# Kernel optimization log

Hardware: AMD Instinct MI355X
Metric: run time of the kernel (lower is better)

## Reference

```python
import jax, jax.numpy as jnp
import numpy as np

EPS = 1e-6
NEG = -1e9
RES_RATIO = 1.0  # res_ratio init arg
MAKE_SYM = True


def _ln(x, g, b):
    m = jnp.mean(x, axis=-1, keepdims=True)
    v = jnp.mean((x - m) ** 2, axis=-1, keepdims=True)
    return (x - m) * jax.lax.rsqrt(v + EPS) * g + b


def _sim(q, k, W1q, W1k, b1, W2, b2):
    # NN(concat([q,k])) with first dense split into query/key halves:
    # relu(q@W1q + k@W1k + b1) @ W2 + b2  -> avoids materializing the 2d concat.
    qa = q @ W1q  # [b,n,sq,h]
    kb = k @ W1k  # [b,n,sk,h]
    h1 = jax.nn.relu(qa[:, :, :, None, :] + kb[:, :, None, :, :] + b1)  # [b,n,sq,sk,h]
    s = jnp.einsum('bnqkh,h->bnqk', h1, W2[:, 0]) + b2[0]
    if MAKE_SYM:
        qb = q @ W1k
        ka = k @ W1q
        h2 = jax.nn.relu(ka[:, :, None, :, :] + qb[:, :, :, None, :] + b1)
        s = s + jnp.einsum('bnqkh,h->bnqk', h2, W2[:, 0]) + b2[0]
    return s


def _attention(v, k, q, mask, Ww, bw, Wd, bd, W1q, W1k, b1, W2, b2):
    q = q @ Ww + bw
    k = k @ Ww + bw
    v = v @ Ww + bw
    logits = _sim(q, k, W1q, W1k, b1, W2, b2)
    if mask is not None:
        logits = logits + mask * NEG
    attn = jax.nn.softmax(logits, axis=-1)
    out = jnp.einsum('bnqk,bnkd->bnqd', attn, v)
    return out @ Wd + bd, attn


def setup_inputs() -> dict:
    key = jax.random.key(0)
    B, N, S, D, DFF, H = 4, 1, 256, 128, 512, 128
    ks = jax.random.split(key, 16)
    s = 0.02
    inp = {
        'x': jax.random.normal(ks[0], (B, N, S, D), jnp.float32),
        'enc_output': jax.random.normal(ks[1], (B, N, S, D), jnp.float32),
        'com_mask': jnp.zeros((B, N, S, S), jnp.float32),
        'dec_mask': jnp.zeros((B, N, S, S), jnp.float32),
        # shared pairwise-score MLP NN: Dense(H, relu) -> Dense(1)
        'W1q': jax.random.normal(ks[2], (D, H), jnp.float32) * s,
        'W1k': jax.random.normal(ks[3], (D, H), jnp.float32) * s,
        'b1': jnp.zeros((H,), jnp.float32),
        'W2': jax.random.normal(ks[4], (H, 1), jnp.float32) * s,
        'b2': jnp.zeros((1,), jnp.float32),
        # mha1 projections
        'Ww1': jax.random.normal(ks[5], (D, D), jnp.float32) * s,
        'bw1': jnp.zeros((D,), jnp.float32),
        'Wd1': jax.random.normal(ks[6], (D, D), jnp.float32) * s,
        'bd1': jnp.zeros((D,), jnp.float32),
        # mha2 projections
        'Ww2': jax.random.normal(ks[7], (D, D), jnp.float32) * s,
        'bw2': jnp.zeros((D,), jnp.float32),
        'Wd2': jax.random.normal(ks[8], (D, D), jnp.float32) * s,
        'bd2': jnp.zeros((D,), jnp.float32),
        # ffn
        'Wf1': jax.random.normal(ks[9], (D, DFF), jnp.float32) * s,
        'bf1': jnp.zeros((DFF,), jnp.float32),
        'Wf2': jax.random.normal(ks[10], (DFF, D), jnp.float32) * s,
        'bf2': jnp.zeros((D,), jnp.float32),
        # layernorms
        'ln1_g': jnp.ones((D,), jnp.float32), 'ln1_b': jnp.zeros((D,), jnp.float32),
        'ln2_g': jnp.ones((D,), jnp.float32), 'ln2_b': jnp.zeros((D,), jnp.float32),
        'ln3_g': jnp.ones((D,), jnp.float32), 'ln3_b': jnp.zeros((D,), jnp.float32),
    }
    return inp


def reference(x, enc_output, com_mask, dec_mask,
              W1q, W1k, b1, W2, b2,
              Ww1, bw1, Wd1, bd1,
              Ww2, bw2, Wd2, bd2,
              Wf1, bf1, Wf2, bf2,
              ln1_g, ln1_b, ln2_g, ln2_b, ln3_g, ln3_b):
    r = RES_RATIO
    # self-attention block (dropout inactive, eval mode)
    attn1, aw1 = _attention(x, x, x, com_mask, Ww1, bw1, Wd1, bd1, W1q, W1k, b1, W2, b2)
    out1 = _ln((2 - r) * attn1 + r * x, ln1_g, ln1_b)
    # cross-attention block
    attn2, aw2 = _attention(enc_output, enc_output, out1, dec_mask, Ww2, bw2, Wd2, bd2, W1q, W1k, b1, W2, b2)
    out2 = _ln((2 - r) * attn2 + r * out1, ln2_g, ln2_b)
    # ffn
    ffn = jax.nn.relu(out2 @ Wf1 + bf1) @ Wf2 + bf2
    out3 = _ln((2 - r) * ffn + r * out2, ln3_g, ln3_b)
    return out3
```

## Files before the change

kernel.cpp:

```cpp
#include <hip/hip_runtime.h>
#include <math.h>


#define LN_EPS 1e-6f
#define NEGV  (-1e9f)

constexpr int B = 4, S = 256, D = 128, H = 128, DFF = 512;
constexpr int R = B * S;

struct P {
    const float *x, *enc, *com_mask, *dec_mask;
    const float *W1q, *W1k, *b1, *W2;
    const float *Ww1, *bw1, *Wd1, *bd1;
    const float *Ww2, *bw2, *Wd2, *bd2;
    const float *Wf1, *bf1, *Wf2, *bf2;
    const float *ln1g, *ln1b, *ln2g, *ln2b, *ln3g, *ln3b;
    float *out;
    float *xw, *qa, *kb, *kv2w, *kb2, *ka2;
};

__global__ __launch_bounds__(512) void proj3_kernel(P p)
{
    const int g = blockIdx.y, tid = threadIdx.x;
    const int r0 = blockIdx.x * 4;
    __shared__ __align__(16) float Ash[4 * 128];
    __shared__ __align__(16) float Pw[4 * 128];
    __shared__ __align__(16) float Pp[4 * 4 * 128];
    __shared__ __align__(16) float P2[2 * 2 * 4 * 128];

    const float* A    = g ? p.enc  : p.x;
    const float* Wp   = g ? p.Ww2  : p.Ww1;
    const float* bp   = g ? p.bw2  : p.bw1;
    float*       o_w  = g ? p.kv2w : p.xw;
    const float* Wsec = g ? p.W1k  : p.W1q;
    const float* bsec = g ? nullptr: p.b1;
    float*       o_s  = g ? p.kb2  : p.qa;
    const float* Wthr = g ? p.W1q  : p.W1k;
    float*       o_t  = g ? p.ka2  : p.kb;

    if (tid < 128)
        ((float4*)Ash)[tid] = ((const float4*)(A + (size_t)r0 * 128))[tid];
    __syncthreads();

    {
        const int kh = tid >> 7, unit = tid & 127, lr = unit >> 5, c4 = unit & 31;
        const float4* W4 = (const float4*)Wp;
        float4 acc = (kh == 0) ? ((const float4*)bp)[c4] : make_float4(0.f, 0.f, 0.f, 0.f);
        const int k0 = kh * 32;
        #pragma unroll 8
        for (int k = 0; k < 32; ++k) {
            const float a = Ash[lr * 128 + k0 + k];
            const float4 w = W4[(k0 + k) * 32 + c4];
            acc.x = fmaf(a, w.x, acc.x); acc.y = fmaf(a, w.y, acc.y);
            acc.z = fmaf(a, w.z, acc.z); acc.w = fmaf(a, w.w, acc.w);
        }
        ((float4*)Pp)[kh * 128 + unit] = acc;
    }
    __syncthreads();
    if (tid < 128) {
        const int lr = tid >> 5, c4 = tid & 31;
        const float4 a0 = ((const float4*)Pp)[tid];
        const float4 a1 = ((const float4*)Pp)[128 + tid];
        const float4 a2 = ((const float4*)Pp)[256 + tid];
        const float4 a3 = ((const float4*)Pp)[384 + tid];
        const float4 w = make_float4(a0.x + a1.x + a2.x + a3.x,
                                     a0.y + a1.y + a2.y + a3.y,
                                     a0.z + a1.z + a2.z + a3.z,
                                     a0.w + a1.w + a2.w + a3.w);
        ((float4*)Pw)[tid] = w;
        ((float4*)o_w)[(size_t)(r0 + lr) * 32 + c4] = w;
    }
    __syncthreads();

    {
        const int which = tid >> 8, sub = tid & 255;
        const int kh = sub >> 7, unit2 = sub & 127, lr = unit2 >> 5, c4 = unit2 & 31;
        const float* W = which ? Wthr : Wsec;
        const float* bb = which ? nullptr : bsec;
        const float4* W4 = (const float4*)W;
        float4 acc = (kh == 0 && bb) ? ((const float4*)bb)[c4]
                                     : make_float4(0.f, 0.f, 0.f, 0.f);
        const int k0 = kh * 64;
        #pragma unroll 8
        for (int k = 0; k < 64; ++k) {
            const float a = Pw[lr * 128 + k0 + k];
            const float4 w = W4[(k0 + k) * 32 + c4];
            acc.x = fmaf(a, w.x, acc.x); acc.y = fmaf(a, w.y, acc.y);
            acc.z = fmaf(a, w.z, acc.z); acc.w = fmaf(a, w.w, acc.w);
        }
        ((float4*)P2)[(which * 2 + kh) * 128 + unit2] = acc;
    }
    __syncthreads();
    if (tid < 256) {
        const int which = tid >> 7, unit2 = tid & 127;
        const int lr = unit2 >> 5, c4 = unit2 & 31;
        const float4 p0 = ((const float4*)P2)[(which * 2 + 0) * 128 + unit2];
        const float4 p1 = ((const float4*)P2)[(which * 2 + 1) * 128 + unit2];
        float* o = which ? o_t : o_s;
        ((float4*)o)[(size_t)(r0 + lr) * 32 + c4] =
            make_float4(p0.x + p1.x, p0.y + p1.y, p0.z + p1.z, p0.w + p1.w);
    }
}

#define SC8(ACC, O1, X1, O2, X2)                                               \
    ACC = fmaf(fmaxf((O1).x + (X1).x, 0.f), w.x, ACC);                         \
    ACC = fmaf(fmaxf((O1).y + (X1).y, 0.f), w.y, ACC);                         \
    ACC = fmaf(fmaxf((O1).z + (X1).z, 0.f), w.z, ACC);                         \
    ACC = fmaf(fmaxf((O1).w + (X1).w, 0.f), w.w, ACC);                         \
    ACC = fmaf(fmaxf((O2).x + (X2).x, 0.f), w.x, ACC);                         \
    ACC = fmaf(fmaxf((O2).y + (X2).y, 0.f), w.y, ACC);                         \
    ACC = fmaf(fmaxf((O2).z + (X2).z, 0.f), w.z, ACC);                         \
    ACC = fmaf(fmaxf((O2).w + (X2).w, 0.f), w.w, ACC);

template<bool FIRST>
__device__ __forceinline__ void attn_stage(const P& p, float* smem,
                                           int tid, int r0, int bS)
{
    float* s8    = smem;
    float* rowS  = smem + 1024;
    float* rinvS = smem + 1536;
    float* qa2L  = smem + 1552;
    float* qb2L  = smem + 2064;
    constexpr int SB = 2576;

    const float* __restrict__ S1g = FIRST ? p.kb : p.kb2;
    const float* __restrict__ S2g = FIRST ? p.qa : p.ka2;
    const float* mask = FIRST ? p.com_mask : p.dec_mask;
    const float* V    = FIRST ? p.xw : p.kv2w;
    const float* Wd   = FIRST ? p.Wd1 : p.Wd2;
    const float* bd   = FIRST ? p.bd1 : p.bd2;
    const float* lg   = FIRST ? p.ln1g : p.ln2g;
    const float* lb   = FIRST ? p.ln1b : p.ln2b;

    {
        const int hh = tid & 7, unit = tid >> 3, kk = unit & 31, rg = unit >> 5;
        const int rA = r0 + 2 * rg, rB = rA + 1;

        float4 o1A[4], o1B[4], o2A[4], o2B[4], w2r[4];
        #pragma unroll
        for (int j = 0; j < 4; ++j) {
            const int h = hh * 4 + 32 * j;
            if (FIRST) {
                o1A[j] = *(const float4*)(p.qa + (size_t)rA * H + h);
                o1B[j] = *(const float4*)(p.qa + (size_t)rB * H + h);
                o2A[j] = *(const float4*)(p.kb + (size_t)rA * H + h);
                o2B[j] = *(const float4*)(p.kb + (size_t)rB * H + h);
            } else {
                o1A[j] = *(const float4*)(qa2L + (2 * rg) * H + h);
                o1B[j] = *(const float4*)(qa2L + (2 * rg + 1) * H + h);
                o2A[j] = *(const float4*)(qb2L + (2 * rg) * H + h);
                o2B[j] = *(const float4*)(qb2L + (2 * rg + 1) * H + h);
            }
            w2r[j] = *(const float4*)(p.W2 + h);
        }

        #pragma unroll
        for (int kt = 0; kt < 4; ++kt) {
            const float* __restrict__ r1a = S1g + (size_t)(bS + kt * 64 + kk)      * H;
            const float* __restrict__ r1b = S1g + (size_t)(bS + kt * 64 + kk + 32) * H;
            const float* __restrict__ r2a = S2g + (size_t)(bS + kt * 64 + kk)      * H;
            const float* __restrict__ r2b = S2g + (size_t)(bS + kt * 64 + kk + 32) * H;

            float4 x1a[4], x1b[4], x2a[4], x2b[4];
            #pragma unroll
            for (int j = 0; j < 4; ++j) {
                const int h = hh * 4 + 32 * j;
                x1a[j] = *(const float4*)(r1a + h);
                x1b[j] = *(const float4*)(r1b + h);
                x2a[j] = *(const float4*)(r2a + h);
                x2b[j] = *(const float4*)(r2b + h);
            }

            float aAa = 0.f, aAb = 0.f, aBa = 0.f, aBb = 0.f;
            #pragma unroll
            for (int j = 0; j < 4; ++j) {
                const float4 w = w2r[j];
                SC8(aAa, o1A[j], x1a[j], o2A[j], x2a[j])
                SC8(aAb, o1A[j], x1b[j], o2A[j], x2b[j])
                SC8(aBa, o1B[j], x1a[j], o2B[j], x2a[j])
                SC8(aBb, o1B[j], x1b[j], o2B[j], x2b[j])
            }
            #pragma unroll
            for (int o = 1; o < 8; o <<= 1) {
                aAa += __shfl_xor(aAa, o, 8);
                aAb += __shfl_xor(aAb, o, 8);
                aBa += __shfl_xor(aBa, o, 8);
                aBb += __shfl_xor(aBb, o, 8);
            }
            if (hh == 0) {
                const int k = kt * 64 + kk;
                s8[(2 * rg) * 256 + k]          = aAa + mask[(size_t)rA * S + k] * NEGV;
                s8[(2 * rg) * 256 + k + 32]     = aAb + mask[(size_t)rA * S + k + 32] * NEGV;
                s8[(2 * rg + 1) * 256 + k]      = aBa + mask[(size_t)rB * S + k] * NEGV;
                s8[(2 * rg + 1) * 256 + k + 32] = aBb + mask[(size_t)rB * S + k + 32] * NEGV;
            }
        }
    }
    __syncthreads();

    {
        const int g = tid >> 6, c = tid & 63;
        if (g < 4) {
            float* rowp = s8 + g * 256;
            float m = -INFINITY;
            #pragma unroll
            for (int k = c; k < 256; k += 64) m = fmaxf(m, rowp[k]);
            for (int o = 32; o; o >>= 1) m = fmaxf(m, __shfl_xor(m, o, 64));
            float s = 0.f;
            #pragma unroll
            for (int k = c; k < 256; k += 64) { const float e = __expf(rowp[k] - m); rowp[k] = e; s += e; }
            for (int o = 32; o; o >>= 1) s += __shfl_xor(s, o, 64);
            if (c == 0) rinvS[g] = 1.f / s;
        }
    }
    __syncthreads();

    float* avp = smem + SB;
    float* aoS = smem + SB + 2048;
    float* pp  = smem + SB + 2560;

    {
        const int r = tid >> 7, t = tid & 127, kq = t >> 5, c4 = t & 31;
        const float4* V4 = (const float4*)(V + (size_t)bS * D);
        const float* sp = s8 + r * 256 + kq * 64;
        float4 acc = make_float4(0.f, 0.f, 0.f, 0.f);
        #pragma unroll 8
        for (int k = 0; k < 64; ++k) {
            const float a = sp[k];
            const float4 v = V4[(kq * 64 + k) * 32 + c4];
            acc.x = fmaf(a, v.x, acc.x); acc.y = fmaf(a, v.y, acc.y);
            acc.z = fmaf(a, v.z, acc.z); acc.w = fmaf(a, v.w, acc.w);
        }
        ((float4*)avp)[(r * 4 + kq) * 32 + c4] = acc;
    }
    __syncthreads();
    if (tid < 128) {
        const int r = tid >> 5, c4 = tid & 31;
        float4 s0 = ((const float4*)avp)[(r * 4 + 0) * 32 + c4];
        const float4 s1 = ((const float4*)avp)[(r * 4 + 1) * 32 + c4];
        const float4 s2 = ((const float4*)avp)[(r * 4 + 2) * 32 + c4];
        const float4 s3 = ((const float4*)avp)[(r * 4 + 3) * 32 + c4];
        const float rv = rinvS[r];
        ((float4*)aoS)[r * 32 + c4] = make_float4(
            (s0.x + s1.x + s2.x + s3.x) * rv, (s0.y + s1.y + s2.y + s3.y) * rv,
            (s0.z + s1.z + s2.z + s3.z) * rv, (s0.w + s1.w + s2.w + s3.w) * rv);
    }
    __syncthreads();

    {
        const int kq = tid >> 7, unit = tid & 127, r = unit >> 5, c4 = unit & 31;
        const float4* W4 = (const float4*)Wd;
        const float* ap = aoS + r * 128 + kq * 32;
        float4 acc = make_float4(0.f, 0.f, 0.f, 0.f);
        #pragma unroll 8
        for (int k = 0; k < 32; ++k) {
            const float a = ap[k];
            const float4 w = W4[(kq * 32 + k) * 32 + c4];
            acc.x = fmaf(a, w.x, acc.x); acc.y = fmaf(a, w.y, acc.y);
            acc.z = fmaf(a, w.z, acc.z); acc.w = fmaf(a, w.w, acc.w);
        }
        ((float4*)pp)[kq * 128 + unit] = acc;
    }
    __syncthreads();

    if (tid < 128) {
        const int r = tid >> 5, c4 = tid & 31;
        const float4 p0 = ((const float4*)pp)[tid];
        const float4 p1 = ((const float4*)pp)[128 + tid];
        const float4 p2 = ((const float4*)pp)[256 + tid];
        const float4 p3 = ((const float4*)pp)[384 + tid];
        const float4 bv0 = ((const float4*)bd)[c4];
        float4 r4;
        if (FIRST) r4 = ((const float4*)(p.x + (size_t)(r0 + r) * 128))[c4];
        else       r4 = ((const float4*)rowS)[r * 32 + c4];
        const float x0 = p0.x + p1.x + p2.x + p3.x + bv0.x + r4.x;
        const float x1 = p0.y + p1.y + p2.y + p3.y + bv0.y + r4.y;
        const float x2 = p0.z + p1.z + p2.z + p3.z + bv0.z + r4.z;
        const float x3 = p0.w + p1.w + p2.w + p3.w + bv0.w + r4.w;
        float s  = x0 + x1 + x2 + x3;
        float s2 = x0 * x0 + x1 * x1 + x2 * x2 + x3 * x3;
        for (int o = 16; o; o >>= 1) { s += __shfl_xor(s, o, 32); s2 += __shfl_xor(s2, o, 32); }
        const float m = s * (1.f / 128), var = s2 * (1.f / 128) - m * m;
        const float rs = rsqrtf(var + LN_EPS);
        const float4 gv = ((const float4*)lg)[c4], bv = ((const float4*)lb)[c4];
        float4 o4;
        o4.x = (x0 - m) * rs * gv.x + bv.x; o4.y = (x1 - m) * rs * gv.y + bv.y;
        o4.z = (x2 - m) * rs * gv.z + bv.z; o4.w = (x3 - m) * rs * gv.w + bv.w;
        ((float4*)rowS)[r * 32 + c4] = o4;
    }
    __syncthreads();

    if (FIRST) {
        float* qpp  = smem + SB;
        float* q2wS = smem + SB + 2048;
        float* qp2  = smem + SB + 2560;
        {
            const int kq = tid >> 7, unit = tid & 127, r = unit >> 5, c4 = unit & 31;
            const float4* W4 = (const float4*)p.Ww2;
            const float* ap = rowS + r * 128 + kq * 32;
            float4 acc = make_float4(0.f, 0.f, 0.f, 0.f);
            #pragma unroll 8
            for (int k = 0; k < 32; ++k) {
                const float a = ap[k];
                const float4 w = W4[(kq * 32 + k) * 32 + c4];
                acc.x = fmaf(a, w.x, acc.x); acc.y = fmaf(a, w.y, acc.y);
                acc.z = fmaf(a, w.z, acc.z); acc.w = fmaf(a, w.w, acc.w);
            }
            ((float4*)qpp)[kq * 128 + unit] = acc;
        }
        __syncthreads();
        if (tid < 128) {
            const int c4 = tid & 31;
            const float4 p0 = ((const float4*)qpp)[tid];
            const float4 p1 = ((const float4*)qpp)[128 + tid];
            const float4 p2 = ((const float4*)qpp)[256 + tid];
            const float4 p3 = ((const float4*)qpp)[384 + tid];
            const float4 bw = ((const float4*)p.bw2)[c4];
            ((float4*)q2wS)[tid] = make_float4(p0.x + p1.x + p2.x + p3.x + bw.x,
                                               p0.y + p1.y + p2.y + p3.y + bw.y,
                                               p0.z + p1.z + p2.z + p3.z + bw.z,
                                               p0.w + p1.w + p2.w + p3.w + bw.w);
        }
        __syncthreads();
        {
            const int which = tid >> 8, sub = tid & 255;
            const int kh = sub >> 7, unit2 = sub & 127;
            const float4* W4 = (const float4*)(which ? p.W1k : p.W1q);
            const int r = unit2 >> 5;
            const float* ap = q2wS + r * 128 + kh * 64;
            float4 acc = make_float4(0.f, 0.f, 0.f, 0.f);
            #pragma unroll 8
            for (int k = 0; k < 64; ++k) {
                const float a = ap[k];
                const float4 w = W4[(kh * 64 + k) * 32 + (unit2 & 31)];
                acc.x = fmaf(a, w.x, acc.x); acc.y = fmaf(a, w.y, acc.y);
                acc.z = fmaf(a, w.z, acc.z); acc.w = fmaf(a, w.w, acc.w);
            }
            ((float4*)qp2)[(which * 2 + kh) * 128 + unit2] = acc;
        }
        __syncthreads();
        if (tid < 256) {
            const int which = tid >> 7, unit2 = tid & 127;
            const int c4 = unit2 & 31;
            const float4 p0 = ((const float4*)qp2)[(which * 2 + 0) * 128 + unit2];
            const float4 p1 = ((const float4*)qp2)[(which * 2 + 1) * 128 + unit2];
            const float4 b1v = ((const float4*)p.b1)[c4];
            float* oq = which ? qb2L : qa2L;
            ((float4*)oq)[unit2] =
                make_float4(p0.x + p1.x + b1v.x, p0.y + p1.y + b1v.y,
                            p0.z + p1.z + b1v.z, p0.w + p1.w + b1v.w);
        }
        __syncthreads();
    } else {
        float* hidP = smem + SB;
        float* part = smem + SB + 8192;
        {
            const int c = tid & 127, kh = tid >> 7;
            const float4* Wf1_4 = (const float4*)p.Wf1;
            float4 a0 = make_float4(0.f,0.f,0.f,0.f), a1 = a0, a2 = a0, a3 = a0;
            const int kbase = kh * 32;
            #pragma unroll 8
            for (int k = 0; k < 32; ++k) {
                const int kk = kbase + k;
                const float4 w = Wf1_4[kk * 128 + c];
                const float s0 = rowS[kk],       s1 = rowS[128 + kk];
                const float s2 = rowS[256 + kk], s3 = rowS[384 + kk];
                a0.x=fmaf(s0,w.x,a0.x); a0.y=fmaf(s0,w.y,a0.y); a0.z=fmaf(s0,w.z,a0.z); a0.w=fmaf(s0,w.w,a0.w);
                a1.x=fmaf(s1,w.x,a1.x); a1.y=fmaf(s1,w.y,a1.y); a1.z=fmaf(s1,w.z,a1.z); a1.w=fmaf(s1,w.w,a1.w);
                a2.x=fmaf(s2,w.x,a2.x); a2.y=fmaf(s2,w.y,a2.y); a2.z=fmaf(s2,w.z,a2.z); a2.w=fmaf(s2,w.w,a2.w);
                a3.x=fmaf(s3,w.x,a3.x); a3.y=fmaf(s3,w.y,a3.y); a3.z=fmaf(s3,w.z,a3.z); a3.w=fmaf(s3,w.w,a3.w);
            }
            float4* h4 = (float4*)hidP;
            const int base = kh * 512;
            h4[base + 0*128 + c] = a0; h4[base + 1*128 + c] = a1;
            h4[base + 2*128 + c] = a2; h4[base + 3*128 + c] = a3;
        }
        __syncthreads();
        for (int i = tid; i < 2048; i += 512) {
            hidP[i] = fmaxf(hidP[i] + hidP[2048 + i] + hidP[4096 + i] + hidP[6144 + i]
                            + p.bf1[i & 511], 0.f);
        }
        __syncthreads();
        {
            const int c4f = tid & 31, kg = tid >> 5;
            const float4* Wf2_4 = (const float4*)p.Wf2;
            float4 a0 = make_float4(0.f,0.f,0.f,0.f), a1 = a0, a2 = a0, a3 = a0;
            const int kbase = kg * 32;
            const float* h0 = hidP + 0 * 512 + kbase;
            const float* h1 = hidP + 1 * 512 + kbase;
            const float* h2 = hidP + 2 * 512 + kbase;
            const float* h3 = hidP + 3 * 512 + kbase;
            #pragma unroll 8
            for (int k = 0; k < 32; ++k) {
                const float4 w = Wf2_4[(kbase + k) * 32 + c4f];
                const float s0 = h0[k], s1 = h1[k], s2 = h2[k], s3 = h3[k];
                a0.x=fmaf(s0,w.x,a0.x); a0.y=fmaf(s0,w.y,a0.y); a0.z=fmaf(s0,w.z,a0.z); a0.w=fmaf(s0,w.w,a0.w);
                a1.x=fmaf(s1,w.x,a1.x); a1.y=fmaf(s1,w.y,a1.y); a1.z=fmaf(s1,w.z,a1.z); a1.w=fmaf(s1,w.w,a1.w);
                a2.x=fmaf(s2,w.x,a2.x); a2.y=fmaf(s2,w.y,a2.y); a2.z=fmaf(s2,w.z,a2.z); a2.w=fmaf(s2,w.w,a2.w);
                a3.x=fmaf(s3,w.x,a3.x); a3.y=fmaf(s3,w.y,a3.y); a3.z=fmaf(s3,w.z,a3.z); a3.w=fmaf(s3,w.w,a3.w);
            }
            float4* p4 = (float4*)part;
            p4[kg * 128 + 0 * 32 + c4f] = a0; p4[kg * 128 + 1 * 32 + c4f] = a1;
            p4[kg * 128 + 2 * 32 + c4f] = a2; p4[kg * 128 + 3 * 32 + c4f] = a3;
        }
        __syncthreads();
        if (tid < 128) {
            const int r = tid >> 5, c4 = tid & 31;
            const float4* p4 = (const float4*)part;
            float4 sum = ((const float4*)p.bf2)[c4];
            #pragma unroll
            for (int kg = 0; kg < 16; ++kg) {
                const float4 v = p4[kg * 128 + r * 32 + c4];
                sum.x += v.x; sum.y += v.y; sum.z += v.z; sum.w += v.w;
            }
            const float4 r4 = ((const float4*)rowS)[r * 32 + c4];
            const float x0 = sum.x + r4.x, x1 = sum.y + r4.y;
            const float x2 = sum.z + r4.z, x3 = sum.w + r4.w;
            float s  = x0 + x1 + x2 + x3;
            float s2 = x0 * x0 + x1 * x1 + x2 * x2 + x3 * x3;
            for (int o = 16; o; o >>= 1) { s += __shfl_xor(s, o, 32); s2 += __shfl_xor(s2, o, 32); }
            const float m = s * (1.f / 128), var = s2 * (1.f / 128) - m * m;
            const float rs = rsqrtf(var + LN_EPS);
            const float4 gv = ((const float4*)p.ln3g)[c4], bv = ((const float4*)p.ln3b)[c4];
            float4 o4;
            o4.x = (x0 - m) * rs * gv.x + bv.x; o4.y = (x1 - m) * rs * gv.y + bv.y;
            o4.z = (x2 - m) * rs * gv.z + bv.z; o4.w = (x3 - m) * rs * gv.w + bv.w;
            ((float4*)p.out)[(size_t)(r0 + r) * 32 + c4] = o4;
        }
    }
}

__global__ __launch_bounds__(512) void fused_attn12_kernel(P p)
{
    __shared__ __align__(16) float smem[18960];
    const int tid = threadIdx.x;
    const int r0 = blockIdx.x * 4, bS = (r0 >> 8) * S;
    attn_stage<true >(p, smem, tid, r0, bS);
    attn_stage<false>(p, smem, tid, r0, bS);
}

extern "C" void kernel_launch(void* const* d_in, const int* in_sizes, int n_in,
                              void* d_out, int out_size, void* d_ws, size_t ws_size,
                              hipStream_t stream) {
    (void)in_sizes; (void)n_in; (void)out_size; (void)ws_size;
    P p;
    p.x        = (const float*)d_in[0];
    p.enc      = (const float*)d_in[1];
    p.com_mask = (const float*)d_in[2];
    p.dec_mask = (const float*)d_in[3];
    p.W1q = (const float*)d_in[4];
    p.W1k = (const float*)d_in[5];
    p.b1  = (const float*)d_in[6];
    p.W2  = (const float*)d_in[7];
    p.Ww1 = (const float*)d_in[9];
    p.bw1 = (const float*)d_in[10];
    p.Wd1 = (const float*)d_in[11];
    p.bd1 = (const float*)d_in[12];
    p.Ww2 = (const float*)d_in[13];
    p.bw2 = (const float*)d_in[14];
    p.Wd2 = (const float*)d_in[15];
    p.bd2 = (const float*)d_in[16];
    p.Wf1 = (const float*)d_in[17];
    p.bf1 = (const float*)d_in[18];
    p.Wf2 = (const float*)d_in[19];
    p.bf2 = (const float*)d_in[20];
    p.ln1g = (const float*)d_in[21];
    p.ln1b = (const float*)d_in[22];
    p.ln2g = (const float*)d_in[23];
    p.ln2b = (const float*)d_in[24];
    p.ln3g = (const float*)d_in[25];
    p.ln3b = (const float*)d_in[26];
    p.out  = (float*)d_out;

    float* ws = (float*)d_ws;
    const size_t RD = (size_t)R * D;
    p.xw    = ws;
    p.qa    = p.xw    + RD;
    p.kb    = p.qa    + RD;
    p.kv2w  = p.kb    + RD;
    p.kb2   = p.kv2w  + RD;
    p.ka2   = p.kb2   + RD;

    proj3_kernel<<<dim3(R / 4, 2), 512, 0, stream>>>(p);
    fused_attn12_kernel<<<R / 4, 512, 0, stream>>>(p);
}
```

Before: 166.1 us.

## Split fused attention kernel into separate score and tail kernels

Splits the single fused two-stage attention kernel into four launches: a score kernel for each attention stage that splits the key dimension across two blocks, and a tail kernel for softmax, PV, projection and LayerNorm. Intermediates (scores, out1, qa2/qb2) now go through global workspace instead of shared memory. The aim is more parallelism for the pairwise-MLP score computation and smaller shared-memory footprints for better occupancy. The cost is extra launches and global round trips for the score matrix and intermediates.

```diff
diff --git a/kernel.cpp b/kernel.cpp
--- a/kernel.cpp
+++ b/kernel.cpp
@@ -16,7 +16,7 @@
     const float *Wf1, *bf1, *Wf2, *bf2;
     const float *ln1g, *ln1b, *ln2g, *ln2b, *ln3g, *ln3b;
     float *out;
-    float *xw, *qa, *kb, *kv2w, *kb2, *ka2;
+    float *xw, *qa, *kb, *kv2w, *kb2, *ka2, *qa2, *qb2, *out1, *sbuf;
 };
 
 __global__ __launch_bounds__(512) void proj3_kernel(P p)
@@ -113,89 +113,96 @@
     ACC = fmaf(fmaxf((O2).w + (X2).w, 0.f), w.w, ACC);
 
 template<bool FIRST>
-__device__ __forceinline__ void attn_stage(const P& p, float* smem,
-                                           int tid, int r0, int bS)
+__global__ __launch_bounds__(512) void score_kernel(P p)
 {
+    const int tid = threadIdx.x;
+    const int r0 = blockIdx.y * 4, bS = (r0 >> 8) * S;
+    const int k0 = blockIdx.x * 128;
+
+    const float* __restrict__ O1g = FIRST ? p.qa : p.qa2;
+    const float* __restrict__ O2g = FIRST ? p.kb : p.qb2;
+    const float* __restrict__ S1g = FIRST ? p.kb : p.kb2;
+    const float* __restrict__ S2g = FIRST ? p.qa : p.ka2;
+    const float* mask = FIRST ? p.com_mask : p.dec_mask;
+
+    const int hh = tid & 7, unit = tid >> 3, kk = unit & 31, rg = unit >> 5;
+    const int rA = r0 + 2 * rg, rB = rA + 1;
+
+    float4 o1A[4], o1B[4], o2A[4], o2B[4], w2r[4];
+    #pragma unroll
+    for (int j = 0; j < 4; ++j) {
+        const int h = hh * 4 + 32 * j;
+        o1A[j] = *(const float4*)(O1g + (size_t)rA * H + h);
+        o1B[j] = *(const float4*)(O1g + (size_t)rB * H + h);
+        o2A[j] = *(const float4*)(O2g + (size_t)rA * H + h);
+        o2B[j] = *(const float4*)(O2g + (size_t)rB * H + h);
+        w2r[j] = *(const float4*)(p.W2 + h);
+    }
+
+    #pragma unroll
+    for (int kt = 0; kt < 2; ++kt) {
+        const int kbase = k0 + kt * 64;
+        const float* __restrict__ r1a = S1g + (size_t)(bS + kbase + kk)      * H;
+        const float* __restrict__ r1b = S1g + (size_t)(bS + kbase + kk + 32) * H;
+        const float* __restrict__ r2a = S2g + (size_t)(bS + kbase + kk)      * H;
+        const float* __restrict__ r2b = S2g + (size_t)(bS + kbase + kk + 32) * H;
+
+        float4 x1a[4], x1b[4], x2a[4], x2b[4];
+        #pragma unroll
+        for (int j = 0; j < 4; ++j) {
+            const int h = hh * 4 + 32 * j;
+            x1a[j] = *(const float4*)(r1a + h);
+            x1b[j] = *(const float4*)(r1b + h);
+            x2a[j] = *(const float4*)(r2a + h);
+            x2b[j] = *(const float4*)(r2b + h);
+        }
+
+        float aAa = 0.f, aAb = 0.f, aBa = 0.f, aBb = 0.f;
+        #pragma unroll
+        for (int j = 0; j < 4; ++j) {
+            const float4 w = w2r[j];
+            SC8(aAa, o1A[j], x1a[j], o2A[j], x2a[j])
+            SC8(aAb, o1A[j], x1b[j], o2A[j], x2b[j])
+            SC8(aBa, o1B[j], x1a[j], o2B[j], x2a[j])
+            SC8(aBb, o1B[j], x1b[j], o2B[j], x2b[j])
+        }
+        #pragma unroll
+        for (int o = 1; o < 8; o <<= 1) {
+            aAa += __shfl_xor(aAa, o, 8);
+            aAb += __shfl_xor(aAb, o, 8);
+            aBa += __shfl_xor(aBa, o, 8);
+            aBb += __shfl_xor(aBb, o, 8);
+        }
+        if (hh == 0) {
+            const int ka = kbase + kk, kbi = kbase + kk + 32;
+            p.sbuf[(size_t)rA * S + ka]  = aAa + mask[(size_t)rA * S + ka]  * NEGV;
+            p.sbuf[(size_t)rA * S + kbi] = aAb + mask[(size_t)rA * S + kbi] * NEGV;
+            p.sbuf[(size_t)rB * S + ka]  = aBa + mask[(size_t)rB * S + ka]  * NEGV;
+            p.sbuf[(size_t)rB * S + kbi] = aBb + mask[(size_t)rB * S + kbi] * NEGV;
+        }
+    }
+}
+
+template<bool FIRST>
+__global__ __launch_bounds__(512) void tail_kernel(P p)
+{
+    __shared__ __align__(16) float smem[FIRST ? 6160 : 17936];
     float* s8    = smem;
     float* rowS  = smem + 1024;
     float* rinvS = smem + 1536;
-    float* qa2L  = smem + 1552;
-    float* qb2L  = smem + 2064;
-    constexpr int SB = 2576;
-
-    const float* __restrict__ S1g = FIRST ? p.kb : p.kb2;
-    const float* __restrict__ S2g = FIRST ? p.qa : p.ka2;
-    const float* mask = FIRST ? p.com_mask : p.dec_mask;
-    const float* V    = FIRST ? p.xw : p.kv2w;
-    const float* Wd   = FIRST ? p.Wd1 : p.Wd2;
-    const float* bd   = FIRST ? p.bd1 : p.bd2;
-    const float* lg   = FIRST ? p.ln1g : p.ln2g;
-    const float* lb   = FIRST ? p.ln1b : p.ln2b;
-
-    {
-        const int hh = tid & 7, unit = tid >> 3, kk = unit & 31, rg = unit >> 5;
-        const int rA = r0 + 2 * rg, rB = rA + 1;
-
-        float4 o1A[4], o1B[4], o2A[4], o2B[4], w2r[4];
-        #pragma unroll
-        for (int j = 0; j < 4; ++j) {
-            const int h = hh * 4 + 32 * j;
-            if (FIRST) {
-                o1A[j] = *(const float4*)(p.qa + (size_t)rA * H + h);
-                o1B[j] = *(const float4*)(p.qa + (size_t)rB * H + h);
-                o2A[j] = *(const float4*)(p.kb + (size_t)rA * H + h);
-                o2B[j] = *(const float4*)(p.kb + (size_t)rB * H + h);
-            } else {
-                o1A[j] = *(const float4*)(qa2L + (2 * rg) * H + h);
-                o1B[j] = *(const float4*)(qa2L + (2 * rg + 1) * H + h);
-                o2A[j] = *(const float4*)(qb2L + (2 * rg) * H + h);
-                o2B[j] = *(const float4*)(qb2L + (2 * rg + 1) * H + h);
-            }
-            w2r[j] = *(const float4*)(p.W2 + h);
-        }
-
-        #pragma unroll
-        for (int kt = 0; kt < 4; ++kt) {
-            const float* __restrict__ r1a = S1g + (size_t)(bS + kt * 64 + kk)      * H;
-            const float* __restrict__ r1b = S1g + (size_t)(bS + kt * 64 + kk + 32) * H;
-            const float* __restrict__ r2a = S2g + (size_t)(bS + kt * 64 + kk)      * H;
-            const float* __restrict__ r2b = S2g + (size_t)(bS + kt * 64 + kk + 32) * H;
-
-            float4 x1a[4], x1b[4], x2a[4], x2b[4];
-            #pragma unroll
-            for (int j = 0; j < 4; ++j) {
-                const int h = hh * 4 + 32 * j;
-                x1a[j] = *(const float4*)(r1a + h);
-                x1b[j] = *(const float4*)(r1b + h);
-                x2a[j] = *(const float4*)(r2a + h);
-                x2b[j] = *(const float4*)(r2b + h);
-            }
-
-            float aAa = 0.f, aAb = 0.f, aBa = 0.f, aBb = 0.f;
-            #pragma unroll
-            for (int j = 0; j < 4; ++j) {
-                const float4 w = w2r[j];
-                SC8(aAa, o1A[j], x1a[j], o2A[j], x2a[j])
-                SC8(aAb, o1A[j], x1b[j], o2A[j], x2b[j])
-                SC8(aBa, o1B[j], x1a[j], o2B[j], x2a[j])
-                SC8(aBb, o1B[j], x1b[j], o2B[j], x2b[j])
-            }
-            #pragma unroll
-            for (int o = 1; o < 8; o <<= 1) {
-                aAa += __shfl_xor(aAa, o, 8);
-                aAb += __shfl_xor(aAb, o, 8);
-                aBa += __shfl_xor(aBa, o, 8);
-                aBb += __shfl_xor(aBb, o, 8);
-            }
-            if (hh == 0) {
-                const int k = kt * 64 + kk;
-                s8[(2 * rg) * 256 + k]          = aAa + mask[(size_t)rA * S + k] * NEGV;
-                s8[(2 * rg) * 256 + k + 32]     = aAb + mask[(size_t)rA * S + k + 32] * NEGV;
-                s8[(2 * rg + 1) * 256 + k]      = aBa + mask[(size_t)rB * S + k] * NEGV;
-                s8[(2 * rg + 1) * 256 + k + 32] = aBb + mask[(size_t)rB * S + k + 32] * NEGV;
-            }
-        }
-    }
+    constexpr int SB = 1552;
+
+    const int tid = threadIdx.x;
+    const int r0 = blockIdx.x * 4, bS = (r0 >> 8) * S;
+
+    const float* V  = FIRST ? p.xw : p.kv2w;
+    const float* Wd = FIRST ? p.Wd1 : p.Wd2;
+    const float* bd = FIRST ? p.bd1 : p.bd2;
+    const float* lg = FIRST ? p.ln1g : p.ln2g;
+    const float* lb = FIRST ? p.ln1b : p.ln2b;
+
+    for (int i = tid; i < 1024; i += 512)
+        s8[i] = p.sbuf[(size_t)(r0 + (i >> 8)) * S + (i & 255)];
     __syncthreads();
 
     {
@@ -270,9 +277,8 @@
         const float4 p2 = ((const float4*)pp)[256 + tid];
         const float4 p3 = ((const float4*)pp)[384 + tid];
         const float4 bv0 = ((const float4*)bd)[c4];
-        float4 r4;
-        if (FIRST) r4 = ((const float4*)(p.x + (size_t)(r0 + r) * 128))[c4];
-        else       r4 = ((const float4*)rowS)[r * 32 + c4];
+        const float* res = FIRST ? p.x : p.out1;
+        const float4 r4 = ((const float4*)(res + (size_t)(r0 + r) * 128))[c4];
         const float x0 = p0.x + p1.x + p2.x + p3.x + bv0.x + r4.x;
         const float x1 = p0.y + p1.y + p2.y + p3.y + bv0.y + r4.y;
         const float x2 = p0.z + p1.z + p2.z + p3.z + bv0.z + r4.z;
@@ -287,6 +293,7 @@
         o4.x = (x0 - m) * rs * gv.x + bv.x; o4.y = (x1 - m) * rs * gv.y + bv.y;
         o4.z = (x2 - m) * rs * gv.z + bv.z; o4.w = (x3 - m) * rs * gv.w + bv.w;
         ((float4*)rowS)[r * 32 + c4] = o4;
+        if (FIRST) ((float4*)p.out1)[(size_t)(r0 + r) * 32 + c4] = o4;
     }
     __syncthreads();
 
@@ -341,16 +348,15 @@
         __syncthreads();
         if (tid < 256) {
             const int which = tid >> 7, unit2 = tid & 127;
-            const int c4 = unit2 & 31;
+            const int r = unit2 >> 5, c4 = unit2 & 31;
             const float4 p0 = ((const float4*)qp2)[(which * 2 + 0) * 128 + unit2];
             const float4 p1 = ((const float4*)qp2)[(which * 2 + 1) * 128 + unit2];
             const float4 b1v = ((const float4*)p.b1)[c4];
-            float* oq = which ? qb2L : qa2L;
-            ((float4*)oq)[unit2] =
+            float* oq = which ? p.qb2 : p.qa2;
+            ((float4*)oq)[(size_t)(r0 + r) * 32 + c4] =
                 make_float4(p0.x + p1.x + b1v.x, p0.y + p1.y + b1v.y,
                             p0.z + p1.z + b1v.z, p0.w + p1.w + b1v.w);
         }
-        __syncthreads();
     } else {
         float* hidP = smem + SB;
         float* part = smem + SB + 8192;
@@ -428,15 +434,6 @@
             ((float4*)p.out)[(size_t)(r0 + r) * 32 + c4] = o4;
         }
     }
-}
-
-__global__ __launch_bounds__(512) void fused_attn12_kernel(P p)
-{
-    __shared__ __align__(16) float smem[18960];
-    const int tid = threadIdx.x;
-    const int r0 = blockIdx.x * 4, bS = (r0 >> 8) * S;
-    attn_stage<true >(p, smem, tid, r0, bS);
-    attn_stage<false>(p, smem, tid, r0, bS);
 }
 
 extern "C" void kernel_launch(void* const* d_in, const int* in_sizes, int n_in,
@@ -473,14 +470,21 @@
     p.out  = (float*)d_out;
 
     float* ws = (float*)d_ws;
-    const size_t RD = (size_t)R * D;
+    const size_t RD  = (size_t)R * D;
     p.xw    = ws;
     p.qa    = p.xw    + RD;
     p.kb    = p.qa    + RD;
     p.kv2w  = p.kb    + RD;
     p.kb2   = p.kv2w  + RD;
     p.ka2   = p.kb2   + RD;
+    p.qa2   = p.ka2   + RD;
+    p.qb2   = p.qa2   + RD;
+    p.out1  = p.qb2   + RD;
+    p.sbuf  = p.out1  + RD;
 
     proj3_kernel<<<dim3(R / 4, 2), 512, 0, stream>>>(p);
-    fused_attn12_kernel<<<R / 4, 512, 0, stream>>>(p);
+    score_kernel<true ><<<dim3(2, R / 4), 512, 0, stream>>>(p);
+    tail_kernel<true ><<<R / 4, 512, 0, stream>>>(p);
+    score_kernel<false><<<dim3(2, R / 4), 512, 0, stream>>>(p);
+    tail_kernel<false><<<R / 4, 512, 0, stream>>>(p);
 }
```

After: 181.5 us. +9.3%, slower.
